# Optimization experiments

Hardware: AMD Instinct MI355X
Metric: run time of the kernel (lower is better)

## Reference

```python
import jax, jax.numpy as jnp
import numpy as np

N_NODES = 100000
N_EDGES = 600000
D_IN = 128
D_OUT = 128


def setup_inputs() -> dict:
    key = jax.random.key(0)
    ks = jax.random.split(key, 8)
    stdv = 1.0 / np.sqrt(D_OUT)
    return {
        "x": jax.random.normal(ks[0], (N_NODES, D_IN), dtype=jnp.float32),
        "edge_src": jax.random.randint(ks[1], (N_EDGES,), 0, N_NODES, dtype=jnp.int32),
        "edge_dst": jax.random.randint(ks[2], (N_EDGES,), 0, N_NODES, dtype=jnp.int32),
        "edge_weight": jax.random.uniform(ks[3], (N_EDGES,), dtype=jnp.float32),
        "weight_l": jax.random.uniform(ks[4], (D_IN, D_OUT), minval=-stdv, maxval=stdv, dtype=jnp.float32),
        "bias_l": jax.random.uniform(ks[5], (D_OUT,), minval=-stdv, maxval=stdv, dtype=jnp.float32),
        "weight_r": jax.random.uniform(ks[6], (D_IN, D_OUT), minval=-stdv, maxval=stdv, dtype=jnp.float32),
        "bias_r": jax.random.uniform(ks[7], (D_OUT,), minval=-stdv, maxval=stdv, dtype=jnp.float32),
    }


def reference(x, edge_src, edge_dst, edge_weight, weight_l, bias_l, weight_r, bias_r):
    # h = input @ weight_l  -> [N, D_OUT]
    h = x @ weight_l
    # spmm(adj, h): out[dst] += adj[dst, src] * h[src]
    msgs = h[edge_src] * edge_weight[:, None]          # [E, D_OUT] gather
    agg = jax.ops.segment_sum(msgs, edge_dst, num_segments=N_NODES)
    out = agg + bias_l
    # root_weight branch (size is None)
    out = out + x @ weight_r + bias_r
    return out
```

## Files before the change

kernel.cpp:

```cpp
#include <hip/hip_runtime.h>
#include <hip/hip_bf16.h>

#define D 128
#define SCAN_BLK 256
#define SCAN_VPT 4
#define SCAN_TILE (SCAN_BLK * SCAN_VPT)

typedef __attribute__((ext_vector_type(8))) short short8;
typedef __attribute__((ext_vector_type(4))) float f32x4;

__global__ __launch_bounds__(256) void prep_w(
    const float* __restrict__ Wl, const float* __restrict__ Wr,
    const float* __restrict__ bl, const float* __restrict__ br,
    __hip_bfloat16* __restrict__ WTl, __hip_bfloat16* __restrict__ WTr,
    float* __restrict__ bsum, int* __restrict__ deg,
    unsigned long long* __restrict__ state, int n_nodes) {
  const int tid = blockIdx.x * 256 + threadIdx.x;
  const int n = (tid >> 7) & 127;
  const int k = tid & 127;
  if (tid < 16384) {
    WTl[n * D + k] = __float2bfloat16(Wl[k * D + n]);
  } else {
    WTr[n * D + k] = __float2bfloat16(Wr[k * D + n]);
  }
  if (tid < 128) bsum[tid] = bl[tid] + br[tid];
  if (tid < 1024) state[tid] = 0ull;
  for (int i = tid; i < n_nodes; i += 32768) deg[i] = 0;
}

__global__ __launch_bounds__(256) void gemm_hr(
    const float* __restrict__ x, const __hip_bfloat16* __restrict__ WTl,
    const __hip_bfloat16* __restrict__ WTr, const float* __restrict__ bsum,
    __hip_bfloat16* __restrict__ h, float* __restrict__ out,
    const int* __restrict__ edst, int* __restrict__ deg, int n_edges) {
  const int t = threadIdx.x;
  const int tid = blockIdx.x * 256 + t;
  if (tid < n_edges) atomicAdd(&deg[edst[tid]], 1);

  __shared__ __hip_bfloat16 xs[32][136];
  const int wave = t >> 6;
  const int lane = t & 63;
  const int m = lane & 15;
  const int q = lane >> 4;
  const int rowbase = blockIdx.x * 32;

  short8 bfl[2][4], bfr[2][4];
  float bias[2];
#pragma unroll
  for (int c = 0; c < 2; ++c) {
    const int n0 = wave * 32 + c * 16;
    bias[c] = bsum[n0 + m];
#pragma unroll
    for (int ks = 0; ks < 4; ++ks) {
      bfl[c][ks] = *(const short8*)&WTl[(n0 + m) * D + ks * 32 + q * 8];
      bfr[c][ks] = *(const short8*)&WTr[(n0 + m) * D + ks * 32 + q * 8];
    }
  }

  const int srow = t >> 3;
  const int scol = (t & 7) * 16;
  {
    const float4* src = (const float4*)&x[(size_t)(rowbase + srow) * D + scol];
    const float4 v0 = src[0], v1 = src[1], v2 = src[2], v3 = src[3];
    __hip_bfloat16* dst = &xs[srow][scol];
    dst[0]  = __float2bfloat16(v0.x); dst[1]  = __float2bfloat16(v0.y);
    dst[2]  = __float2bfloat16(v0.z); dst[3]  = __float2bfloat16(v0.w);
    dst[4]  = __float2bfloat16(v1.x); dst[5]  = __float2bfloat16(v1.y);
    dst[6]  = __float2bfloat16(v1.z); dst[7]  = __float2bfloat16(v1.w);
    dst[8]  = __float2bfloat16(v2.x); dst[9]  = __float2bfloat16(v2.y);
    dst[10] = __float2bfloat16(v2.z); dst[11] = __float2bfloat16(v2.w);
    dst[12] = __float2bfloat16(v3.x); dst[13] = __float2bfloat16(v3.y);
    dst[14] = __float2bfloat16(v3.z); dst[15] = __float2bfloat16(v3.w);
  }
  __syncthreads();

  f32x4 aL[2][2], aR[2][2];
#pragma unroll
  for (int hf = 0; hf < 2; ++hf)
#pragma unroll
    for (int c = 0; c < 2; ++c)
#pragma unroll
      for (int r = 0; r < 4; ++r) { aL[hf][c][r] = 0.f; aR[hf][c][r] = 0.f; }

#pragma unroll
  for (int hf = 0; hf < 2; ++hf) {
#pragma unroll
    for (int ks = 0; ks < 4; ++ks) {
      const short8 afrag = *(const short8*)&xs[hf * 16 + m][ks * 32 + q * 8];
#pragma unroll
      for (int c = 0; c < 2; ++c) {
        aL[hf][c] = __builtin_amdgcn_mfma_f32_16x16x32_bf16(afrag, bfl[c][ks], aL[hf][c], 0, 0, 0);
        aR[hf][c] = __builtin_amdgcn_mfma_f32_16x16x32_bf16(afrag, bfr[c][ks], aR[hf][c], 0, 0, 0);
      }
    }
  }
  __syncthreads();

#pragma unroll
  for (int hf = 0; hf < 2; ++hf) {
#pragma unroll
    for (int c = 0; c < 2; ++c) {
      const int n = wave * 32 + c * 16 + m;
#pragma unroll
      for (int r = 0; r < 4; ++r) {
        const int row = hf * 16 + q * 4 + r;
        out[(size_t)(rowbase + row) * D + n] = aR[hf][c][r] + bias[c];
        xs[row][n] = __float2bfloat16(aL[hf][c][r]);
      }
    }
  }
  __syncthreads();

  *(short8*)&h[(size_t)(rowbase + srow) * D + scol] = *(const short8*)&xs[srow][scol];
  *(short8*)&h[(size_t)(rowbase + srow) * D + scol + 8] = *(const short8*)&xs[srow][scol + 8];
}

__global__ __launch_bounds__(SCAN_BLK) void scan_ll(
    int* __restrict__ pos , int* __restrict__ offsets,
    unsigned long long* __restrict__ state, int n, int n_edges) {
  __shared__ int sdata[SCAN_BLK];
  __shared__ int s_prefix;
  const int t = threadIdx.x;
  const int b = blockIdx.x;
  const int base = b * SCAN_TILE + t * SCAN_VPT;

  int v[SCAN_VPT];
  int s = 0;
#pragma unroll
  for (int j = 0; j < SCAN_VPT; ++j) {
    v[j] = (base + j < n) ? pos[base + j] : 0;
    s += v[j];
  }
  sdata[t] = s;
  __syncthreads();
  for (int off = 1; off < SCAN_BLK; off <<= 1) {
    int xv = (t >= off) ? sdata[t - off] : 0;
    __syncthreads();
    sdata[t] += xv;
    __syncthreads();
  }
  const int excl = sdata[t] - s;
  const int total = sdata[SCAN_BLK - 1];

  if (t == 0) {
    const unsigned long long st =
        ((unsigned long long)(b == 0 ? 2 : 1) << 62) | (unsigned int)total;
    __hip_atomic_store(&state[b], st, __ATOMIC_RELEASE, __HIP_MEMORY_SCOPE_AGENT);
  }

  if (b == 0) {
    if (t == 0) s_prefix = 0;
  } else if (t < 64) {
    int windowEnd = b;
    int acc = 0;
    for (;;) {
      const int j = windowEnd - 1 - t;
      unsigned long long st = 0;
      if (j >= 0) {
        do {
          st = __hip_atomic_load(&state[j], __ATOMIC_ACQUIRE, __HIP_MEMORY_SCOPE_AGENT);
        } while (st == 0);
      }
      const int flag = (j >= 0) ? (int)(st >> 62) : 2;
      const int val = (j >= 0) ? (int)(st & 0xffffffffull) : 0;
      const unsigned long long mask = __ballot(flag == 2);
      if (mask) {
        const int firstLane = __ffsll((long long)mask) - 1;
        int contrib = (t <= firstLane) ? val : 0;
#pragma unroll
        for (int o = 32; o > 0; o >>= 1) contrib += __shfl_down(contrib, o);
        if (t == 0) { acc += contrib; s_prefix = acc; }
        break;
      } else {
        int contrib = val;
#pragma unroll
        for (int o = 32; o > 0; o >>= 1) contrib += __shfl_down(contrib, o);
        if (t == 0) acc += contrib;
        windowEnd -= 64;
      }
    }
  }
  __syncthreads();
  const int add = s_prefix;

  if (t == 0 && b > 0) {
    const unsigned long long st =
        (2ull << 62) | (unsigned int)(add + total);
    __hip_atomic_store(&state[b], st, __ATOMIC_RELEASE, __HIP_MEMORY_SCOPE_AGENT);
  }

  int run = add + excl;
#pragma unroll
  for (int j = 0; j < SCAN_VPT; ++j) {
    if (base + j < n) {
      offsets[base + j] = run;
      pos[base + j] = run;
    }
    run += v[j];
  }
  if (b == 0 && t == 0) offsets[n] = n_edges;
}

__global__ __launch_bounds__(256) void scatter_kernel(
    const int* __restrict__ esrc, const int* __restrict__ edst,
    const float* __restrict__ ew, int* __restrict__ pos,
    int2* __restrict__ pairs, int n_edges) {
  const int e = blockIdx.x * 256 + threadIdx.x;
  if (e >= n_edges) return;
  const int d = edst[e];
  const int slot = atomicAdd(&pos[d], 1);
  pairs[slot] = make_int2(esrc[e], __float_as_int(ew[e]));
}

__global__ __launch_bounds__(256) void sage_agg(
    const __hip_bfloat16* __restrict__ h,
    const int* __restrict__ offsets, const int2* __restrict__ pairs,
    float* __restrict__ out, int n_nodes) {
  const int node = blockIdx.x * 4 + (threadIdx.x >> 6);
  const int lane = threadIdx.x & 63;
  if (node >= n_nodes) return;
  const int begin = offsets[node];
  const int end = offsets[node + 1];
  const __hip_bfloat162* __restrict__ h2 = (const __hip_bfloat162*)h;

  float2 a = *(const float2*)&out[(size_t)node * D + 2 * lane];

  int i = begin;
  for (; i + 8 <= end; i += 8) {
    int2 p[8];
#pragma unroll
    for (int u = 0; u < 8; ++u) p[u] = pairs[i + u];
    __hip_bfloat162 hv[8];
#pragma unroll
    for (int u = 0; u < 8; ++u)
      hv[u] = h2[(size_t)p[u].x * (D / 2) + lane];
#pragma unroll
    for (int u = 0; u < 8; ++u) {
      const float w = __int_as_float(p[u].y);
      a.x = fmaf(w, __bfloat162float(hv[u].x), a.x);
      a.y = fmaf(w, __bfloat162float(hv[u].y), a.y);
    }
  }
  if (i < end) {
    int2 p[8];
#pragma unroll
    for (int u = 0; u < 8; ++u) {
      const int ei = (i + u < end) ? (i + u) : (end - 1);
      p[u] = pairs[ei];
      if (i + u >= end) p[u].y = 0;
    }
    __hip_bfloat162 hv[8];
#pragma unroll
    for (int u = 0; u < 8; ++u)
      hv[u] = h2[(size_t)p[u].x * (D / 2) + lane];
#pragma unroll
    for (int u = 0; u < 8; ++u) {
      const float w = __int_as_float(p[u].y);
      a.x = fmaf(w, __bfloat162float(hv[u].x), a.x);
      a.y = fmaf(w, __bfloat162float(hv[u].y), a.y);
    }
  }

  *(float2*)&out[(size_t)node * D + 2 * lane] = a;
}

extern "C" void kernel_launch(void* const* d_in, const int* in_sizes, int n_in,
                              void* d_out, int out_size, void* d_ws, size_t ws_size,
                              hipStream_t stream) {
  const float* x   = (const float*)d_in[0];
  const int* esrc  = (const int*)d_in[1];
  const int* edst  = (const int*)d_in[2];
  const float* ew  = (const float*)d_in[3];
  const float* Wl  = (const float*)d_in[4];
  const float* bl  = (const float*)d_in[5];
  const float* Wr  = (const float*)d_in[6];
  const float* br  = (const float*)d_in[7];
  float* out = (float*)d_out;

  const int n_nodes = in_sizes[0] / D;
  const int n_edges = in_sizes[1];

  char* ws = (char*)d_ws;
  size_t off = 0;
  __hip_bfloat16* h = (__hip_bfloat16*)(ws + off);
  off += (size_t)n_nodes * D * sizeof(__hip_bfloat16);
  off = (off + 15) & ~15ull;
  int* offsets = (int*)(ws + off);
  off += (size_t)(n_nodes + 1) * sizeof(int);
  off = (off + 15) & ~15ull;
  int* pos = (int*)(ws + off);
  off += (size_t)n_nodes * sizeof(int);
  off = (off + 15) & ~15ull;
  unsigned long long* state = (unsigned long long*)(ws + off);
  off += 1024 * sizeof(unsigned long long);
  off = (off + 15) & ~15ull;
  int2* pairs = (int2*)(ws + off);
  off += (size_t)n_edges * sizeof(int2);
  off = (off + 15) & ~15ull;
  __hip_bfloat16* WTl = (__hip_bfloat16*)(ws + off);
  off += (size_t)D * D * sizeof(__hip_bfloat16);
  __hip_bfloat16* WTr = (__hip_bfloat16*)(ws + off);
  off += (size_t)D * D * sizeof(__hip_bfloat16);
  float* bsum = (float*)(ws + off);
  off += D * sizeof(float);

  prep_w<<<128, 256, 0, stream>>>(Wl, Wr, bl, br, WTl, WTr, bsum, pos, state, n_nodes);

  const int n_tiles32 = (n_nodes + 31) / 32;
  gemm_hr<<<n_tiles32, 256, 0, stream>>>(x, WTl, WTr, bsum, h, out, edst, pos, n_edges);

  const int nparts = (n_nodes + SCAN_TILE - 1) / SCAN_TILE;
  scan_ll<<<nparts, SCAN_BLK, 0, stream>>>(pos, offsets, state, n_nodes, n_edges);

  scatter_kernel<<<(n_edges + 255) / 256, 256, 0, stream>>>(esrc, edst, ew, pos, pairs, n_edges);

  sage_agg<<<(n_nodes + 3) / 4, 256, 0, stream>>>(h, offsets, pairs, out, n_nodes);
}
```

Measured before the change: 239.8 us.

## Use per-wave GEMM tiles without LDS and aggregate two nodes per wave

The GEMM kernel now gives each wave its own 16-row tile. It loads x directly from global memory into registers as bf16 MFMA fragments and loops over all 128 output columns, writing h and out straight from the accumulators. This removes the LDS staging and the barriers, but it gives up coalesced stores and reloads the weight fragments per wave. The aggregation kernel now has each wave handle two consecutive nodes over one merged edge range, which evens out the partial-batch tail and raises memory parallelism for low-degree nodes. In exchange it adds predicated FMAs for the node that does not own each edge.

```diff
diff --git a/kernel.cpp b/kernel.cpp
--- a/kernel.cpp
+++ b/kernel.cpp
@@ -8,6 +8,11 @@
 
 typedef __attribute__((ext_vector_type(8))) short short8;
 typedef __attribute__((ext_vector_type(4))) float f32x4;
+
+static __device__ __forceinline__ short f2bs(float f) {
+  __hip_bfloat16 b = __float2bfloat16(f);
+  return *reinterpret_cast<short*>(&b);
+}
 
 __global__ __launch_bounds__(256) void prep_w(
     const float* __restrict__ Wl, const float* __restrict__ Wr,
@@ -28,91 +33,67 @@
   for (int i = tid; i < n_nodes; i += 32768) deg[i] = 0;
 }
 
-__global__ __launch_bounds__(256) void gemm_hr(
+__global__ __launch_bounds__(256) void gemm_wt(
     const float* __restrict__ x, const __hip_bfloat16* __restrict__ WTl,
     const __hip_bfloat16* __restrict__ WTr, const float* __restrict__ bsum,
     __hip_bfloat16* __restrict__ h, float* __restrict__ out,
-    const int* __restrict__ edst, int* __restrict__ deg, int n_edges) {
+    const int* __restrict__ edst, int* __restrict__ deg, int n_edges,
+    int n_tiles) {
   const int t = threadIdx.x;
-  const int tid = blockIdx.x * 256 + t;
-  if (tid < n_edges) atomicAdd(&deg[edst[tid]], 1);
-
-  __shared__ __hip_bfloat16 xs[32][136];
-  const int wave = t >> 6;
+  const int gsz = gridDim.x * 256;
+  for (int e = blockIdx.x * 256 + t; e < n_edges; e += gsz)
+    atomicAdd(&deg[edst[e]], 1);
+
+  const int wtile = blockIdx.x * 4 + (t >> 6);
+  if (wtile >= n_tiles) return;
   const int lane = t & 63;
   const int m = lane & 15;
   const int q = lane >> 4;
-  const int rowbase = blockIdx.x * 32;
-
-  short8 bfl[2][4], bfr[2][4];
-  float bias[2];
-#pragma unroll
-  for (int c = 0; c < 2; ++c) {
-    const int n0 = wave * 32 + c * 16;
-    bias[c] = bsum[n0 + m];
+  const int rowbase = wtile * 16;
+
+  const float* __restrict__ xrow = &x[(size_t)(rowbase + m) * D];
+  float4 av[4][2];
+#pragma unroll
+  for (int ks = 0; ks < 4; ++ks) {
+    av[ks][0] = *(const float4*)&xrow[ks * 32 + q * 8];
+    av[ks][1] = *(const float4*)&xrow[ks * 32 + q * 8 + 4];
+  }
+  short8 afrag[4];
+#pragma unroll
+  for (int ks = 0; ks < 4; ++ks) {
+    short8 f;
+    f[0] = f2bs(av[ks][0].x); f[1] = f2bs(av[ks][0].y);
+    f[2] = f2bs(av[ks][0].z); f[3] = f2bs(av[ks][0].w);
+    f[4] = f2bs(av[ks][1].x); f[5] = f2bs(av[ks][1].y);
+    f[6] = f2bs(av[ks][1].z); f[7] = f2bs(av[ks][1].w);
+    afrag[ks] = f;
+  }
+
+#pragma unroll 2
+  for (int c = 0; c < 8; ++c) {
+    const int n0 = c * 16;
+    short8 bfl[4], bfr[4];
 #pragma unroll
     for (int ks = 0; ks < 4; ++ks) {
-      bfl[c][ks] = *(const short8*)&WTl[(n0 + m) * D + ks * 32 + q * 8];
-      bfr[c][ks] = *(const short8*)&WTr[(n0 + m) * D + ks * 32 + q * 8];
-    }
-  }
-
-  const int srow = t >> 3;
-  const int scol = (t & 7) * 16;
-  {
-    const float4* src = (const float4*)&x[(size_t)(rowbase + srow) * D + scol];
-    const float4 v0 = src[0], v1 = src[1], v2 = src[2], v3 = src[3];
-    __hip_bfloat16* dst = &xs[srow][scol];
-    dst[0]  = __float2bfloat16(v0.x); dst[1]  = __float2bfloat16(v0.y);
-    dst[2]  = __float2bfloat16(v0.z); dst[3]  = __float2bfloat16(v0.w);
-    dst[4]  = __float2bfloat16(v1.x); dst[5]  = __float2bfloat16(v1.y);
-    dst[6]  = __float2bfloat16(v1.z); dst[7]  = __float2bfloat16(v1.w);
-    dst[8]  = __float2bfloat16(v2.x); dst[9]  = __float2bfloat16(v2.y);
-    dst[10] = __float2bfloat16(v2.z); dst[11] = __float2bfloat16(v2.w);
-    dst[12] = __float2bfloat16(v3.x); dst[13] = __float2bfloat16(v3.y);
-    dst[14] = __float2bfloat16(v3.z); dst[15] = __float2bfloat16(v3.w);
-  }
-  __syncthreads();
-
-  f32x4 aL[2][2], aR[2][2];
-#pragma unroll
-  for (int hf = 0; hf < 2; ++hf)
-#pragma unroll
-    for (int c = 0; c < 2; ++c)
-#pragma unroll
-      for (int r = 0; r < 4; ++r) { aL[hf][c][r] = 0.f; aR[hf][c][r] = 0.f; }
-
-#pragma unroll
-  for (int hf = 0; hf < 2; ++hf) {
+      bfl[ks] = *(const short8*)&WTl[(n0 + m) * D + ks * 32 + q * 8];
+      bfr[ks] = *(const short8*)&WTr[(n0 + m) * D + ks * 32 + q * 8];
+    }
+    f32x4 aL, aR;
+#pragma unroll
+    for (int r = 0; r < 4; ++r) { aL[r] = 0.f; aR[r] = 0.f; }
 #pragma unroll
     for (int ks = 0; ks < 4; ++ks) {
-      const short8 afrag = *(const short8*)&xs[hf * 16 + m][ks * 32 + q * 8];
-#pragma unroll
-      for (int c = 0; c < 2; ++c) {
-        aL[hf][c] = __builtin_amdgcn_mfma_f32_16x16x32_bf16(afrag, bfl[c][ks], aL[hf][c], 0, 0, 0);
-        aR[hf][c] = __builtin_amdgcn_mfma_f32_16x16x32_bf16(afrag, bfr[c][ks], aR[hf][c], 0, 0, 0);
-      }
-    }
-  }
-  __syncthreads();
-
-#pragma unroll
-  for (int hf = 0; hf < 2; ++hf) {
-#pragma unroll
-    for (int c = 0; c < 2; ++c) {
-      const int n = wave * 32 + c * 16 + m;
-#pragma unroll
-      for (int r = 0; r < 4; ++r) {
-        const int row = hf * 16 + q * 4 + r;
-        out[(size_t)(rowbase + row) * D + n] = aR[hf][c][r] + bias[c];
-        xs[row][n] = __float2bfloat16(aL[hf][c][r]);
-      }
-    }
-  }
-  __syncthreads();
-
-  *(short8*)&h[(size_t)(rowbase + srow) * D + scol] = *(const short8*)&xs[srow][scol];
-  *(short8*)&h[(size_t)(rowbase + srow) * D + scol + 8] = *(const short8*)&xs[srow][scol + 8];
+      aL = __builtin_amdgcn_mfma_f32_16x16x32_bf16(afrag[ks], bfl[ks], aL, 0, 0, 0);
+      aR = __builtin_amdgcn_mfma_f32_16x16x32_bf16(afrag[ks], bfr[ks], aR, 0, 0, 0);
+    }
+    const float bias = bsum[n0 + m];
+#pragma unroll
+    for (int r = 0; r < 4; ++r) {
+      const size_t row = (size_t)(rowbase + q * 4 + r);
+      h[row * D + n0 + m] = __float2bfloat16(aL[r]);
+      out[row * D + n0 + m] = aR[r] + bias;
+    }
+  }
 }
 
 __global__ __launch_bounds__(SCAN_BLK) void scan_ll(
@@ -184,8 +165,7 @@
   const int add = s_prefix;
 
   if (t == 0 && b > 0) {
-    const unsigned long long st =
-        (2ull << 62) | (unsigned int)(add + total);
+    const unsigned long long st = (2ull << 62) | (unsigned int)(add + total);
     __hip_atomic_store(&state[b], st, __ATOMIC_RELEASE, __HIP_MEMORY_SCOPE_AGENT);
   }
 
@@ -216,52 +196,51 @@
     const __hip_bfloat16* __restrict__ h,
     const int* __restrict__ offsets, const int2* __restrict__ pairs,
     float* __restrict__ out, int n_nodes) {
-  const int node = blockIdx.x * 4 + (threadIdx.x >> 6);
+  const int wid = blockIdx.x * 4 + (threadIdx.x >> 6);
+  const int node0 = wid * 2;
+  if (node0 >= n_nodes) return;
   const int lane = threadIdx.x & 63;
-  if (node >= n_nodes) return;
-  const int begin = offsets[node];
-  const int end = offsets[node + 1];
+  const bool two = (node0 + 1 < n_nodes);
+
+  float2 a0 = *(const float2*)&out[(size_t)node0 * D + 2 * lane];
+  float2 a1 = two ? *(const float2*)&out[(size_t)(node0 + 1) * D + 2 * lane]
+                  : make_float2(0.f, 0.f);
+
+  const int b0 = offsets[node0];
+  const int e0 = offsets[node0 + 1];
+  const int e1 = two ? offsets[node0 + 2] : e0;
   const __hip_bfloat162* __restrict__ h2 = (const __hip_bfloat162*)h;
 
-  float2 a = *(const float2*)&out[(size_t)node * D + 2 * lane];
-
-  int i = begin;
-  for (; i + 8 <= end; i += 8) {
+  for (int i = b0; i < e1; i += 8) {
     int2 p[8];
-#pragma unroll
-    for (int u = 0; u < 8; ++u) p[u] = pairs[i + u];
+    float wv[8];
+#pragma unroll
+    for (int u = 0; u < 8; ++u) {
+      const int idx = i + u;
+      const int ci = idx < e1 ? idx : e1 - 1;
+      p[u] = pairs[ci];
+      wv[u] = (idx < e1) ? __int_as_float(p[u].y) : 0.f;
+    }
     __hip_bfloat162 hv[8];
 #pragma unroll
     for (int u = 0; u < 8; ++u)
       hv[u] = h2[(size_t)p[u].x * (D / 2) + lane];
 #pragma unroll
     for (int u = 0; u < 8; ++u) {
-      const float w = __int_as_float(p[u].y);
-      a.x = fmaf(w, __bfloat162float(hv[u].x), a.x);
-      a.y = fmaf(w, __bfloat162float(hv[u].y), a.y);
-    }
-  }
-  if (i < end) {
-    int2 p[8];
-#pragma unroll
-    for (int u = 0; u < 8; ++u) {
-      const int ei = (i + u < end) ? (i + u) : (end - 1);
-      p[u] = pairs[ei];
-      if (i + u >= end) p[u].y = 0;
-    }
-    __hip_bfloat162 hv[8];
-#pragma unroll
-    for (int u = 0; u < 8; ++u)
-      hv[u] = h2[(size_t)p[u].x * (D / 2) + lane];
-#pragma unroll
-    for (int u = 0; u < 8; ++u) {
-      const float w = __int_as_float(p[u].y);
-      a.x = fmaf(w, __bfloat162float(hv[u].x), a.x);
-      a.y = fmaf(w, __bfloat162float(hv[u].y), a.y);
-    }
-  }
-
-  *(float2*)&out[(size_t)node * D + 2 * lane] = a;
+      const bool to0 = (i + u) < e0;
+      const float w0 = to0 ? wv[u] : 0.f;
+      const float w1 = to0 ? 0.f : wv[u];
+      const float hx = __bfloat162float(hv[u].x);
+      const float hy = __bfloat162float(hv[u].y);
+      a0.x = fmaf(w0, hx, a0.x);
+      a0.y = fmaf(w0, hy, a0.y);
+      a1.x = fmaf(w1, hx, a1.x);
+      a1.y = fmaf(w1, hy, a1.y);
+    }
+  }
+
+  *(float2*)&out[(size_t)node0 * D + 2 * lane] = a0;
+  if (two) *(float2*)&out[(size_t)(node0 + 1) * D + 2 * lane] = a1;
 }
 
 extern "C" void kernel_launch(void* const* d_in, const int* in_sizes, int n_in,
@@ -306,13 +285,16 @@
 
   prep_w<<<128, 256, 0, stream>>>(Wl, Wr, bl, br, WTl, WTr, bsum, pos, state, n_nodes);
 
-  const int n_tiles32 = (n_nodes + 31) / 32;
-  gemm_hr<<<n_tiles32, 256, 0, stream>>>(x, WTl, WTr, bsum, h, out, edst, pos, n_edges);
+  const int n_tiles = (n_nodes + 15) / 16;
+  const int gemm_blocks = (n_tiles + 3) / 4;
+  gemm_wt<<<gemm_blocks, 256, 0, stream>>>(x, WTl, WTr, bsum, h, out, edst, pos,
+                                           n_edges, n_tiles);
 
   const int nparts = (n_nodes + SCAN_TILE - 1) / SCAN_TILE;
   scan_ll<<<nparts, SCAN_BLK, 0, stream>>>(pos, offsets, state, n_nodes, n_edges);
 
   scatter_kernel<<<(n_edges + 255) / 256, 256, 0, stream>>>(esrc, edst, ew, pos, pairs, n_edges);
 
-  sage_agg<<<(n_nodes + 3) / 4, 256, 0, stream>>>(h, offsets, pairs, out, n_nodes);
-}
+  const int agg_blocks = (n_nodes / 2 + 3) / 4;
+  sage_agg<<<agg_blocks, 256, 0, stream>>>(h, offsets, pairs, out, n_nodes);
+}
```

After: 267.2 us. +11.4%, slower.

## Make GEMM kernel persistent with 16-row tiles and register prefetch of next tile

Applied to the files above, without the earlier changes.

The projection GEMM kernel now runs as a grid-stride persistent kernel capped at 2048 blocks. Each block processes 16-row tiles and prefetches the next tile's x rows into registers while computing the current one. Weight fragments are loaded once per block instead of once per tile. The h output is now written directly from MFMA accumulators as scattered bf16 stores rather than staged through shared memory for vectorized stores, which may reduce store coalescing. The degree-count atomics also move to a grid-stride loop.

```diff
diff --git a/kernel.cpp b/kernel.cpp
--- a/kernel.cpp
+++ b/kernel.cpp
@@ -32,17 +32,18 @@
     const float* __restrict__ x, const __hip_bfloat16* __restrict__ WTl,
     const __hip_bfloat16* __restrict__ WTr, const float* __restrict__ bsum,
     __hip_bfloat16* __restrict__ h, float* __restrict__ out,
-    const int* __restrict__ edst, int* __restrict__ deg, int n_edges) {
+    const int* __restrict__ edst, int* __restrict__ deg, int n_edges,
+    int n_rowtiles) {
   const int t = threadIdx.x;
-  const int tid = blockIdx.x * 256 + t;
-  if (tid < n_edges) atomicAdd(&deg[edst[tid]], 1);
-
-  __shared__ __hip_bfloat16 xs[32][136];
+  const int gsz = gridDim.x * 256;
+  for (int e = blockIdx.x * 256 + t; e < n_edges; e += gsz)
+    atomicAdd(&deg[edst[e]], 1);
+
+  __shared__ __hip_bfloat16 xs[16][136];
   const int wave = t >> 6;
   const int lane = t & 63;
   const int m = lane & 15;
   const int q = lane >> 4;
-  const int rowbase = blockIdx.x * 32;
 
   short8 bfl[2][4], bfr[2][4];
   float bias[2];
@@ -57,62 +58,64 @@
     }
   }
 
-  const int srow = t >> 3;
-  const int scol = (t & 7) * 16;
-  {
-    const float4* src = (const float4*)&x[(size_t)(rowbase + srow) * D + scol];
-    const float4 v0 = src[0], v1 = src[1], v2 = src[2], v3 = src[3];
-    __hip_bfloat16* dst = &xs[srow][scol];
-    dst[0]  = __float2bfloat16(v0.x); dst[1]  = __float2bfloat16(v0.y);
-    dst[2]  = __float2bfloat16(v0.z); dst[3]  = __float2bfloat16(v0.w);
-    dst[4]  = __float2bfloat16(v1.x); dst[5]  = __float2bfloat16(v1.y);
-    dst[6]  = __float2bfloat16(v1.z); dst[7]  = __float2bfloat16(v1.w);
-    dst[8]  = __float2bfloat16(v2.x); dst[9]  = __float2bfloat16(v2.y);
-    dst[10] = __float2bfloat16(v2.z); dst[11] = __float2bfloat16(v2.w);
-    dst[12] = __float2bfloat16(v3.x); dst[13] = __float2bfloat16(v3.y);
-    dst[14] = __float2bfloat16(v3.z); dst[15] = __float2bfloat16(v3.w);
-  }
-  __syncthreads();
-
-  f32x4 aL[2][2], aR[2][2];
-#pragma unroll
-  for (int hf = 0; hf < 2; ++hf)
+  const int srow = t >> 4;
+  const int scol = (t & 15) * 8;
+
+  int rt = blockIdx.x;
+  float4 pv0, pv1;
+  if (rt < n_rowtiles) {
+    const float4* src = (const float4*)&x[(size_t)(rt * 16 + srow) * D + scol];
+    pv0 = src[0];
+    pv1 = src[1];
+  }
+
+  for (; rt < n_rowtiles; rt += gridDim.x) {
+    const int rowbase = rt * 16;
+
+    {
+      __hip_bfloat16* dst = &xs[srow][scol];
+      dst[0] = __float2bfloat16(pv0.x); dst[1] = __float2bfloat16(pv0.y);
+      dst[2] = __float2bfloat16(pv0.z); dst[3] = __float2bfloat16(pv0.w);
+      dst[4] = __float2bfloat16(pv1.x); dst[5] = __float2bfloat16(pv1.y);
+      dst[6] = __float2bfloat16(pv1.z); dst[7] = __float2bfloat16(pv1.w);
+    }
+    __syncthreads();
+
+    const int nrt = rt + gridDim.x;
+    if (nrt < n_rowtiles) {
+      const float4* src = (const float4*)&x[(size_t)(nrt * 16 + srow) * D + scol];
+      pv0 = src[0];
+      pv1 = src[1];
+    }
+
+    f32x4 accL[2], accR[2];
 #pragma unroll
     for (int c = 0; c < 2; ++c)
 #pragma unroll
-      for (int r = 0; r < 4; ++r) { aL[hf][c][r] = 0.f; aR[hf][c][r] = 0.f; }
-
-#pragma unroll
-  for (int hf = 0; hf < 2; ++hf) {
+      for (int r = 0; r < 4; ++r) { accL[c][r] = 0.f; accR[c][r] = 0.f; }
+
 #pragma unroll
     for (int ks = 0; ks < 4; ++ks) {
-      const short8 afrag = *(const short8*)&xs[hf * 16 + m][ks * 32 + q * 8];
+      const short8 afrag = *(const short8*)&xs[m][ks * 32 + q * 8];
 #pragma unroll
       for (int c = 0; c < 2; ++c) {
-        aL[hf][c] = __builtin_amdgcn_mfma_f32_16x16x32_bf16(afrag, bfl[c][ks], aL[hf][c], 0, 0, 0);
-        aR[hf][c] = __builtin_amdgcn_mfma_f32_16x16x32_bf16(afrag, bfr[c][ks], aR[hf][c], 0, 0, 0);
+        accL[c] = __builtin_amdgcn_mfma_f32_16x16x32_bf16(afrag, bfl[c][ks], accL[c], 0, 0, 0);
+        accR[c] = __builtin_amdgcn_mfma_f32_16x16x32_bf16(afrag, bfr[c][ks], accR[c], 0, 0, 0);
       }
     }
-  }
-  __syncthreads();
-
-#pragma unroll
-  for (int hf = 0; hf < 2; ++hf) {
+
 #pragma unroll
     for (int c = 0; c < 2; ++c) {
       const int n = wave * 32 + c * 16 + m;
 #pragma unroll
       for (int r = 0; r < 4; ++r) {
-        const int row = hf * 16 + q * 4 + r;
-        out[(size_t)(rowbase + row) * D + n] = aR[hf][c][r] + bias[c];
-        xs[row][n] = __float2bfloat16(aL[hf][c][r]);
+        const size_t row = (size_t)(rowbase + q * 4 + r);
+        h[row * D + n] = __float2bfloat16(accL[c][r]);
+        out[row * D + n] = accR[c][r] + bias[c];
       }
     }
-  }
-  __syncthreads();
-
-  *(short8*)&h[(size_t)(rowbase + srow) * D + scol] = *(const short8*)&xs[srow][scol];
-  *(short8*)&h[(size_t)(rowbase + srow) * D + scol + 8] = *(const short8*)&xs[srow][scol + 8];
+    __syncthreads();
+  }
 }
 
 __global__ __launch_bounds__(SCAN_BLK) void scan_ll(
@@ -184,8 +187,7 @@
   const int add = s_prefix;
 
   if (t == 0 && b > 0) {
-    const unsigned long long st =
-        (2ull << 62) | (unsigned int)(add + total);
+    const unsigned long long st = (2ull << 62) | (unsigned int)(add + total);
     __hip_atomic_store(&state[b], st, __ATOMIC_RELEASE, __HIP_MEMORY_SCOPE_AGENT);
   }
 
@@ -306,8 +308,10 @@
 
   prep_w<<<128, 256, 0, stream>>>(Wl, Wr, bl, br, WTl, WTr, bsum, pos, state, n_nodes);
 
-  const int n_tiles32 = (n_nodes + 31) / 32;
-  gemm_hr<<<n_tiles32, 256, 0, stream>>>(x, WTl, WTr, bsum, h, out, edst, pos, n_edges);
+  const int n_rowtiles = (n_nodes + 15) / 16;
+  const int gemm_grid = n_rowtiles < 2048 ? n_rowtiles : 2048;
+  gemm_hr<<<gemm_grid, 256, 0, stream>>>(x, WTl, WTr, bsum, h, out, edst, pos,
+                                         n_edges, n_rowtiles);
 
   const int nparts = (n_nodes + SCAN_TILE - 1) / SCAN_TILE;
   scan_ll<<<nparts, SCAN_BLK, 0, stream>>>(pos, offsets, state, n_nodes, n_edges);
```

After: 242.6 us. No clear change (+1.2%).
